# Optimization experiments

Measured on AMD Instinct MI355X. Metric: run time of the kernel, lower is better.

## Reference

```python
import jax, jax.numpy as jnp
import numpy as np

WORD, D, H = 512, 64, 8  # word_size, embed_dim (per-head), n_query

def setup_inputs() -> dict:
    key = jax.random.key(0)
    ks = jax.random.split(key, 9)
    B, S = 2, 4096
    sw = 1.0 / np.sqrt(WORD)
    x  = jax.random.normal(ks[0], (B, S, WORD), dtype=jnp.float32)
    Wk = jax.random.normal(ks[1], (WORD, D), dtype=jnp.float32) * sw
    bk = jnp.zeros((D,), jnp.float32)
    Wv = jax.random.normal(ks[2], (WORD, D), dtype=jnp.float32) * sw
    bv = jnp.zeros((D,), jnp.float32)
    Wq = jax.random.normal(ks[3], (H, WORD, D), dtype=jnp.float32) * sw
    bq = jnp.zeros((H, D), jnp.float32)
    Wp = jax.random.normal(ks[4], (H * D, D), dtype=jnp.float32) * (1.0 / np.sqrt(H * D))
    bp = jnp.zeros((D,), jnp.float32)
    return {"x": x, "Wq": Wq, "bq": bq, "Wk": Wk, "bk": bk, "Wv": Wv, "bv": bv, "Wp": Wp, "bp": bp}

def reference(x, Wq, bq, Wk, bk, Wv, bv, Wp, bp):
    # shared K/V across all query heads (multi-query attention)
    K = x @ Wk + bk                                   # [b, s, d]
    V = x @ Wv + bv                                   # [b, s, d]
    Q = jnp.einsum('bsw,hwd->bhsd', x, Wq) + bq[None, :, None, :]  # [b, h, s, d]
    scale = 1.0 / jnp.sqrt(jnp.float32(D))
    scores = jnp.einsum('bhsd,btd->bhst', Q, K) * scale  # [b, h, s, t]
    attn = jax.nn.softmax(scores, axis=-1)
    Z = jnp.einsum('bhst,btd->bhsd', attn, V)            # [b, h, s, d]
    B, _, S, _ = Z.shape
    Zc = jnp.transpose(Z, (0, 2, 1, 3)).reshape(B, S, H * D)  # concat heads
    return Zc @ Wp + bp                                   # [b, s, d]
```

## Files before the change

### kernel.cpp

```cpp
#include <hip/hip_runtime.h>
#include <hip/hip_bf16.h>
#include <stdint.h>

#define BB 2
#define SS 4096
#define WW 512
#define DD 64
#define HH 8
#define QSCALE 0.1803368801111244f

typedef __hip_bfloat16 bf16;
typedef __bf16 bf16x8 __attribute__((ext_vector_type(8)));
typedef float f32x16 __attribute__((ext_vector_type(16)));
typedef unsigned int u32x4 __attribute__((ext_vector_type(4)));
typedef unsigned int u32x2 __attribute__((ext_vector_type(2)));

union U4 { u32x4 u4; unsigned int u[4]; bf16x8 v; };

__device__ __forceinline__ float ldv(const float* p, size_t i) { return p[i]; }
__device__ __forceinline__ float ldv(const bf16* p, size_t i)  { return __bfloat162float(p[i]); }

__device__ __forceinline__ unsigned short f2bu(float f) {
    union Ub { bf16 b; unsigned short u; } t;
    t.b = __float2bfloat16(f);
    return t.u;
}

__device__ __forceinline__ float fast_exp2(float x) {
#if __has_builtin(__builtin_amdgcn_exp2f)
    return __builtin_amdgcn_exp2f(x);
#else
    return exp2f(x);
#endif
}

__device__ __forceinline__ f32x16 mfma_bf16(bf16x8 a, bf16x8 b, f32x16 c) {
    return __builtin_amdgcn_mfma_f32_32x32x16_bf16(a, b, c, 0, 0, 0);
}

__device__ __forceinline__ unsigned int pk_bf16(float lo, float hi) {
    unsigned int a = __float_as_uint(lo) + 0x8000u;
    unsigned int b = __float_as_uint(hi) + 0x8000u;
    return __builtin_amdgcn_perm(b, a, 0x07060302u);
}

__device__ __forceinline__ unsigned int cvtpk_bf16(float lo, float hi) {
    unsigned int r;
    asm("v_cvt_pk_bf16_f32 %0, %1, %2" : "=v"(r) : "v"(lo), "v"(hi));
    return r;
}

__device__ __forceinline__ int block_detect(const void* raw, int* cntLds)
{
    if (threadIdx.x == 0) *cntLds = 0;
    __syncthreads();
    const bf16* xb = (const bf16*)raw;
    const float v = __bfloat162float(xb[2 * threadIdx.x]);
    const float a = fabsf(v);
    const bool insane = !(v == v) || (a >= 1.0e4f) || (a != 0.0f && a <= 1.0e-8f);
    const unsigned long long m = __ballot(insane);
    if ((threadIdx.x & 63) == 0) atomicAdd(cntLds, __popcll(m));
    __syncthreads();
    return (*cntLds * 2 > 256) ? 1 : 0;
}

template<typename T>
__device__ __forceinline__ void prep_w_body(
    const T* Wq, const T* bq, const T* Wk, const T* bk,
    const T* Wv, const T* bv, const T* Wp, const T* bp,
    unsigned short* Wb, float* bb, float (*Tt)[65], int pwblk)
{
    const int tid = threadIdx.x;
    const int cg = pwblk >> 3, wg = pwblk & 7;
    const int c0 = cg * 64, w0 = wg * 64;
    const T* src = (cg == 0) ? Wk : (cg == 1) ? Wv
                 : (cg == 10) ? Wp : (Wq + (size_t)(cg - 2) * WW * DD);
    const float scale = (cg >= 2 && cg < 10) ? QSCALE : 1.0f;

    #pragma unroll
    for (int i = 0; i < 16; ++i) {
        const int e = i * 256 + tid, w = e >> 6, d = e & 63;
        Tt[w][d] = ldv(src, (size_t)(w0 + w) * DD + d) * scale;
    }
    __syncthreads();
    #pragma unroll
    for (int i = 0; i < 16; ++i) {
        const int e = i * 256 + tid, d = e >> 6, w = e & 63;
        Wb[(size_t)(c0 + d) * WW + w0 + w] = f2bu(Tt[w][d]);
    }
    if (pwblk == 0) {
        #pragma unroll
        for (int i = 0; i < 3; ++i) {
            const int c = tid + i * 256;
            if (c < 704) {
                float v;
                if (c < 64)       v = ldv(bk, c);
                else if (c < 128) v = ldv(bv, c - 64);
                else if (c < 640) v = ldv(bq, c - 128) * QSCALE;
                else              v = ldv(bp, c - 640);
                bb[c] = v;
            }
        }
    }
}

__global__ __launch_bounds__(256) void prep_kernel(
    const void* x, const void* Wq, const void* bq, const void* Wk, const void* bk,
    const void* Wv, const void* bv, const void* Wp, const void* bp,
    unsigned short* xb, unsigned short* Wb, float* bb, int* flag)
{
    __shared__ float Tt[64][65];
    __shared__ int cnt;
    const int blk = blockIdx.x;

    if (blk < 2048) {
        const int fl = block_detect(x, &cnt);
        if (blk == 0 && threadIdx.x == 0) *flag = fl;
        const size_t i = ((size_t)blk * 256 + threadIdx.x) * 8;
        if (fl) {
            const float4* p = (const float4*)((const float*)x + i);
            const float4 a = p[0], b = p[1];
            unsigned int w[4];
            w[0] = pk_bf16(a.x, a.y); w[1] = pk_bf16(a.z, a.w);
            w[2] = pk_bf16(b.x, b.y); w[3] = pk_bf16(b.z, b.w);
            *(u32x4*)(xb + i) = *(u32x4*)w;
        } else {
            *(u32x4*)(xb + i) = *(const u32x4*)((const unsigned short*)x + i);
        }
    } else {
        const int fl = block_detect(Wk, &cnt);
        if (fl)
            prep_w_body<float>((const float*)Wq, (const float*)bq, (const float*)Wk,
                               (const float*)bk, (const float*)Wv, (const float*)bv,
                               (const float*)Wp, (const float*)bp, Wb, bb, Tt, blk - 2048);
        else
            prep_w_body<bf16>((const bf16*)Wq, (const bf16*)bq, (const bf16*)Wk,
                              (const bf16*)bk, (const bf16*)Wv, (const bf16*)bv,
                              (const bf16*)Wp, (const bf16*)bp, Wb, bb, Tt, blk - 2048);
    }
}

#define KP 40

__global__ __launch_bounds__(256, 2) void proj_mfma_kernel(
    const unsigned short* __restrict__ xb, const unsigned short* __restrict__ Wb,
    const float* __restrict__ bb,
    bf16* __restrict__ Kb, unsigned short* __restrict__ Vtg, bf16* __restrict__ Qb)
{
    __shared__ unsigned short As[2][128 * KP];
    __shared__ unsigned short Bs[2][128 * KP];

    const int tid = threadIdx.x;
    const int wv = tid >> 6, ln = tid & 63;
    const int g = ln >> 5, cc = ln & 31;
    const int nblk = blockIdx.x % 5, mblk = blockIdx.x / 5;
    const int row0 = mblk * 128, n0 = nblk * 128;
    const int wm = (wv & 1) * 64, wn = (wv >> 1) * 64;

    const int sm = tid >> 2;
    const int sko = (tid & 3) * 8;

    u32x4 pa[2], pb[2];
    #define GLOAD(kt)                                                          \
        do {                                                                   \
            _Pragma("unroll")                                                  \
            for (int i = 0; i < 2; ++i) {                                      \
                const int m = sm + i * 64;                                     \
                pa[i] = *(const u32x4*)&xb[(size_t)(row0 + m) * WW + (kt) * 32 + sko]; \
                pb[i] = *(const u32x4*)&Wb[(size_t)(n0 + m) * WW + (kt) * 32 + sko];   \
            }                                                                  \
        } while (0)
    #define LWRITE(buf)                                                        \
        do {                                                                   \
            _Pragma("unroll")                                                  \
            for (int i = 0; i < 2; ++i) {                                      \
                const int m = sm + i * 64;                                     \
                *(u32x4*)&As[buf][m * KP + sko] = pa[i];                       \
                *(u32x4*)&Bs[buf][m * KP + sko] = pb[i];                       \
            }                                                                  \
        } while (0)

    f32x16 acc[2][2];
    #pragma unroll
    for (int a = 0; a < 2; ++a)
        #pragma unroll
        for (int c2 = 0; c2 < 2; ++c2)
            #pragma unroll
            for (int i = 0; i < 16; ++i) acc[a][c2][i] = 0.f;

    GLOAD(0); LWRITE(0);
    GLOAD(1);

    for (int kt = 0; kt < 16; ++kt) {
        __syncthreads();
        const int buf = kt & 1;
        #pragma unroll
        for (int ks = 0; ks < 2; ++ks) {
            U4 af[2], bfr[2];
            #pragma unroll
            for (int ms = 0; ms < 2; ++ms)
                af[ms].u4 = *(const u32x4*)&As[buf][(wm + ms * 32 + cc) * KP + ks * 16 + g * 8];
            #pragma unroll
            for (int ns = 0; ns < 2; ++ns)
                bfr[ns].u4 = *(const u32x4*)&Bs[buf][(wn + ns * 32 + cc) * KP + ks * 16 + g * 8];
            #pragma unroll
            for (int ms = 0; ms < 2; ++ms)
                #pragma unroll
                for (int ns = 0; ns < 2; ++ns)
                    acc[ms][ns] = mfma_bf16(af[ms].v, bfr[ns].v, acc[ms][ns]);
        }
        if (kt < 15) {
            LWRITE(buf ^ 1);
            if (kt < 14) GLOAD(kt + 2);
        }
    }
    #undef GLOAD
    #undef LWRITE

    const int b = row0 >> 12;
    #pragma unroll
    for (int ns = 0; ns < 2; ++ns) {
        const int c = n0 + wn + ns * 32 + cc;
        const int grp = c >> 6, d = c & 63;
        const float bias = bb[c];
        if (grp == 1) {
            unsigned short* vt = Vtg + ((size_t)(b * DD + d)) * SS;
            #pragma unroll
            for (int ms = 0; ms < 2; ++ms) {
                #pragma unroll
                for (int reg = 0; reg < 16; ++reg) {
                    const int r = (reg & 3) + 8 * (reg >> 2) + 4 * g;
                    const int lrow = (row0 & 4095) + wm + ms * 32 + r;
                    const int srow = (lrow & ~12) | ((lrow & 4) << 1) | ((lrow & 8) >> 1);
                    vt[srow] = f2bu(acc[ms][ns][reg] + bias);
                }
            }
        } else {
            bf16* base = (grp == 0) ? Kb
                       : Qb + (size_t)((b * HH + grp - 2) - b) * SS * DD;
            #pragma unroll
            for (int ms = 0; ms < 2; ++ms) {
                #pragma unroll
                for (int reg = 0; reg < 16; ++reg) {
                    const int r = (reg & 3) + 8 * (reg >> 2) + 4 * g;
                    const int row = row0 + wm + ms * 32 + r;
                    base[(size_t)row * DD + d] = __float2bfloat16(acc[ms][ns][reg] + bias);
                }
            }
        }
    }
}

#define VTP 72
#define ZP_PART ((size_t)16 * 64 * 4096)
#define LP_PART ((size_t)16 * 4096)

template<int TSPLIT>
__global__ __launch_bounds__(256, 2) void attn_mfma_kernel(
    const bf16* __restrict__ Kb, const unsigned short* __restrict__ Vtg,
    const bf16* __restrict__ Qb, bf16* __restrict__ Zb,
    float* __restrict__ Zp, float* __restrict__ Lp)
{
    __shared__ unsigned short Vt[2][64 * VTP];
    __shared__ unsigned short Kt[2][64 * VTP];

    const int tid = threadIdx.x;
    const int wv = tid >> 6, ln = tid & 63;
    const int g  = ln >> 5, cc = ln & 31;
    constexpr int TSB = (TSPLIT == 1) ? 0 : 1;
    const int chunk = blockIdx.x & 15;
    const int tsp = (blockIdx.x >> 4) & (TSPLIT - 1);
    const int bh  = blockIdx.x >> (4 + TSB);
    const int b = bh >> 3, h = bh & 7;
    const int qw = chunk * 256 + wv * 64;
    const int it0 = tsp * (64 / TSPLIT);
    const int itN = it0 + 64 / TSPLIT;

    const unsigned short* Kg = (const unsigned short*)(Kb + (size_t)b * SS * DD);
    const unsigned short* Vg = Vtg + (size_t)b * DD * SS;
    const char* Qg = (const char*)(Qb + (size_t)(b * HH + h) * SS * DD);

    const int sr = tid >> 2, sc = (tid & 3) * 16;
    const unsigned short* VgRow = Vg + (size_t)sr * SS;

    U4 qf[2][4];
    #pragma unroll
    for (int nt = 0; nt < 2; ++nt)
        #pragma unroll
        for (int ks = 0; ks < 4; ++ks)
            qf[nt][ks].u4 = *(const u32x4*)(Qg +
                (size_t)((qw + nt * 32 + cc) * 64 + g * 8 + ks * 16) * 2);

    const f32x16 fzero = {0.f, 0.f, 0.f, 0.f, 0.f, 0.f, 0.f, 0.f,
                          0.f, 0.f, 0.f, 0.f, 0.f, 0.f, 0.f, 0.f};
    U4 ones;
    ones.u[0] = 0x3F803F80u; ones.u[1] = 0x3F803F80u;
    ones.u[2] = 0x3F803F80u; ones.u[3] = 0x3F803F80u;

    f32x16 zacc[2][2];
    #pragma unroll
    for (int nt = 0; nt < 2; ++nt)
        #pragma unroll
        for (int dt = 0; dt < 2; ++dt)
            #pragma unroll
            for (int i = 0; i < 16; ++i) zacc[nt][dt][i] = 0.f;

    f32x16 lacc[2];
    #pragma unroll
    for (int nt = 0; nt < 2; ++nt)
        #pragma unroll
        for (int i = 0; i < 16; ++i) lacc[nt][i] = 0.f;

    {
        const unsigned short* ksrc = Kg + (size_t)(it0 * 64 + sr) * 64 + sc;
        const unsigned short* vsrc = VgRow + it0 * 64 + sc;
        *(u32x4*)&Kt[0][sr * VTP + sc + 0] = *(const u32x4*)&ksrc[0];
        *(u32x4*)&Kt[0][sr * VTP + sc + 8] = *(const u32x4*)&ksrc[8];
        *(u32x4*)&Vt[0][sr * VTP + sc + 0] = *(const u32x4*)&vsrc[0];
        *(u32x4*)&Vt[0][sr * VTP + sc + 8] = *(const u32x4*)&vsrc[8];
    }

    for (int it = it0; it < itN; ++it) {
        __syncthreads();
        const int buf = it & 1;
        const bool more = (it + 1) < itN;
        u32x4 pk0, pk1, pv0, pv1;
        if (more) {
            const unsigned short* ksrc = Kg + (size_t)((it + 1) * 64 + sr) * 64 + sc;
            const unsigned short* vsrc = VgRow + (it + 1) * 64 + sc;
            pk0 = *(const u32x4*)&ksrc[0];
            pk1 = *(const u32x4*)&ksrc[8];
            pv0 = *(const u32x4*)&vsrc[0];
            pv1 = *(const u32x4*)&vsrc[8];
        }

        #pragma unroll
        for (int si = 0; si < 2; ++si) {
            U4 kf[4];
            #pragma unroll
            for (int ks = 0; ks < 4; ++ks)
                kf[ks].u4 = *(const u32x4*)&Kt[buf][(si * 32 + cc) * VTP +
                                                    ks * 16 + g * 8];
            U4 vf[2][2];
            #pragma unroll
            for (int ks = 0; ks < 2; ++ks)
                #pragma unroll
                for (int dt = 0; dt < 2; ++dt)
                    vf[ks][dt].u4 = *(const u32x4*)&Vt[buf][(dt * 32 + cc) * VTP +
                                                            si * 32 + ks * 16 + g * 8];

            #pragma unroll
            for (int nt = 0; nt < 2; ++nt) {
                __builtin_amdgcn_s_setprio(1);
                f32x16 s = mfma_bf16(kf[0].v, qf[nt][0].v, fzero);
                #pragma unroll
                for (int ks = 1; ks < 4; ++ks) s = mfma_bf16(kf[ks].v, qf[nt][ks].v, s);
                __builtin_amdgcn_s_setprio(0);

                float p[16];
                #pragma unroll
                for (int i = 0; i < 16; ++i) p[i] = fast_exp2(s[i]);
                unsigned int w0[8];
                #pragma unroll
                for (int i2 = 0; i2 < 8; ++i2)
                    w0[i2] = cvtpk_bf16(p[2 * i2], p[2 * i2 + 1]);

                __builtin_amdgcn_s_setprio(1);
                #pragma unroll
                for (int ks = 0; ks < 2; ++ks) {
                    U4 pb;
                    pb.u[0] = w0[ks * 4 + 0]; pb.u[1] = w0[ks * 4 + 1];
                    pb.u[2] = w0[ks * 4 + 2]; pb.u[3] = w0[ks * 4 + 3];
                    lacc[nt] = mfma_bf16(ones.v, pb.v, lacc[nt]);
                    #pragma unroll
                    for (int dt = 0; dt < 2; ++dt)
                        zacc[nt][dt] = mfma_bf16(vf[ks][dt].v, pb.v, zacc[nt][dt]);
                }
                __builtin_amdgcn_s_setprio(0);
            }
        }

        if (more) {
            *(u32x4*)&Kt[buf ^ 1][sr * VTP + sc + 0] = pk0;
            *(u32x4*)&Kt[buf ^ 1][sr * VTP + sc + 8] = pk1;
            *(u32x4*)&Vt[buf ^ 1][sr * VTP + sc + 0] = pv0;
            *(u32x4*)&Vt[buf ^ 1][sr * VTP + sc + 8] = pv1;
        }
    }

    float l[2];
    l[0] = lacc[0][0];
    l[1] = lacc[1][0];

    if (TSPLIT == 1) {
        #pragma unroll
        for (int nt = 0; nt < 2; ++nt) {
            const float rr = 1.0f / l[nt];
            bf16* zp = Zb + (size_t)(b * SS + qw + nt * 32 + cc) * (HH * DD)
                     + h * DD + g * 4;
            #pragma unroll
            for (int dt = 0; dt < 2; ++dt)
                #pragma unroll
                for (int i = 0; i < 16; ++i) {
                    const int d = (i & 3) + 8 * (i >> 2) + 32 * dt;
                    zp[d] = __float2bfloat16(zacc[nt][dt][i] * rr);
                }
        }
    } else {
        float* zp0 = Zp + (size_t)(tsp * 16 + bh) * (64 * 4096);
        #pragma unroll
        for (int nt = 0; nt < 2; ++nt) {
            const int q = qw + nt * 32 + cc;
            #pragma unroll
            for (int dt = 0; dt < 2; ++dt)
                #pragma unroll
                for (int i = 0; i < 16; ++i) {
                    const int d = (i & 3) + 8 * (i >> 2) + 4 * g + 32 * dt;
                    zp0[(size_t)d * 4096 + q] = zacc[nt][dt][i];
                }
            if (g == 0)
                Lp[(size_t)(tsp * 16 + bh) * 4096 + q] = l[nt];
        }
    }
}

template<int NP>
__global__ __launch_bounds__(256) void combine_kernel(
    const float* __restrict__ Zp, const float* __restrict__ Lp,
    bf16* __restrict__ Zb)
{
    const size_t T = (size_t)blockIdx.x * 256 + threadIdx.x;
    const int sblk = (int)(T & 511);
    const int d  = (int)((T >> 9) & 63);
    const int bh = (int)(T >> 15);
    const int s0 = sblk * 8;
    const int b = bh >> 3, h = bh & 7;

    const float* p0 = Zp + ((size_t)bh * 64 + d) * 4096 + s0;
    const float* l0 = Lp + (size_t)bh * 4096 + s0;

    float z[8], lv[8];
    #pragma unroll
    for (int j = 0; j < 8; ++j) { z[j] = 0.f; lv[j] = 0.f; }
    #pragma unroll
    for (int np = 0; np < NP; ++np) {
        const float* p = p0 + (size_t)np * ZP_PART;
        const float* l = l0 + (size_t)np * LP_PART;
        #pragma unroll
        for (int j = 0; j < 8; j += 4) {
            const float4 a = *(const float4*)(p + j);
            z[j] += a.x; z[j+1] += a.y; z[j+2] += a.z; z[j+3] += a.w;
            const float4 e = *(const float4*)(l + j);
            lv[j] += e.x; lv[j+1] += e.y; lv[j+2] += e.z; lv[j+3] += e.w;
        }
    }
    bf16* zo = Zb + ((size_t)(b * SS + s0)) * (HH * DD) + h * DD + d;
    #pragma unroll
    for (int j = 0; j < 8; ++j)
        zo[(size_t)j * (HH * DD)] = __float2bfloat16(z[j] / lv[j]);
}

__global__ __launch_bounds__(256) void outp_mfma_kernel(
    const bf16* __restrict__ Zb, const unsigned short* __restrict__ Wb,
    const float* __restrict__ bb, const int* flag, void* out)
{
    __shared__ unsigned short As[2][128 * KP];
    __shared__ unsigned short Bs[2][64 * KP];

    const int tid = threadIdx.x;
    const int wv = tid >> 6, ln = tid & 63;
    const int g = ln >> 5, cc = ln & 31;
    const int row0 = blockIdx.x * 128;
    const int sm = tid >> 2, sko = (tid & 3) * 8;

    const unsigned short* Zu = (const unsigned short*)Zb;
    const unsigned short* Wn = Wb + (size_t)640 * WW;
    const float* bbp = bb + 640;

    u32x4 pa[2], pbv;
    #define GLOAD2(kt)                                                         \
        do {                                                                   \
            _Pragma("unroll")                                                  \
            for (int i = 0; i < 2; ++i)                                        \
                pa[i] = *(const u32x4*)&Zu[(size_t)(row0 + sm + i * 64) * WW + (kt) * 32 + sko]; \
            pbv = *(const u32x4*)&Wn[(size_t)sm * WW + (kt) * 32 + sko];       \
        } while (0)
    #define LWRITE2(buf)                                                       \
        do {                                                                   \
            _Pragma("unroll")                                                  \
            for (int i = 0; i < 2; ++i)                                        \
                *(u32x4*)&As[buf][(sm + i * 64) * KP + sko] = pa[i];           \
            *(u32x4*)&Bs[buf][sm * KP + sko] = pbv;                            \
        } while (0)

    f32x16 acc[2];
    #pragma unroll
    for (int ns = 0; ns < 2; ++ns)
        #pragma unroll
        for (int i = 0; i < 16; ++i) acc[ns][i] = 0.f;

    GLOAD2(0); LWRITE2(0);
    GLOAD2(1);

    for (int kt = 0; kt < 16; ++kt) {
        __syncthreads();
        const int buf = kt & 1;
        #pragma unroll
        for (int ks = 0; ks < 2; ++ks) {
            U4 af;
            af.u4 = *(const u32x4*)&As[buf][(wv * 32 + cc) * KP + ks * 16 + g * 8];
            #pragma unroll
            for (int ns = 0; ns < 2; ++ns) {
                U4 bf2;
                bf2.u4 = *(const u32x4*)&Bs[buf][(ns * 32 + cc) * KP + ks * 16 + g * 8];
                acc[ns] = mfma_bf16(af.v, bf2.v, acc[ns]);
            }
        }
        if (kt < 15) {
            LWRITE2(buf ^ 1);
            if (kt < 14) GLOAD2(kt + 2);
        }
    }
    #undef GLOAD2
    #undef LWRITE2

    const int fl = *flag;
    #pragma unroll
    for (int ns = 0; ns < 2; ++ns) {
        const int c = ns * 32 + cc;
        const float bias = bbp[c];
        #pragma unroll
        for (int reg = 0; reg < 16; ++reg) {
            const int r = (reg & 3) + 8 * (reg >> 2) + 4 * g;
            const int row = row0 + wv * 32 + r;
            const float v = acc[ns][reg] + bias;
            if (fl) ((float*)out)[(size_t)row * DD + c] = v;
            else    ((bf16*)out)[(size_t)row * DD + c] = __float2bfloat16(v);
        }
    }
}

extern "C" void kernel_launch(void* const* d_in, const int* in_sizes, int n_in,
                              void* d_out, int out_size, void* d_ws, size_t ws_size,
                              hipStream_t stream)
{
    const void* x  = d_in[0];
    const void* Wq = d_in[1];
    const void* bq = d_in[2];
    const void* Wk = d_in[3];
    const void* bk = d_in[4];
    const void* Wv = d_in[5];
    const void* bv = d_in[6];
    const void* Wp = d_in[7];
    const void* bp = d_in[8];

    char* ws = (char*)d_ws;
    bf16* Kb = (bf16*)(ws);
    bf16* Qb = (bf16*)(ws + (2u << 20));
    bf16* Zb = (bf16*)(ws + (10u << 20));
    unsigned short* xb = (unsigned short*)(ws + (10u << 20));
    int* flag = (int*)(ws + (18u << 20));
    unsigned short* Wb = (unsigned short*)(ws + (18u << 20) + 64);
    float* bb = (float*)(ws + (18u << 20) + 64 + 704 * 512 * 2);
    unsigned short* Vtg = (unsigned short*)(ws + (19u << 20));
    float* Zp = (float*)(ws + (20u << 20));
    float* Lp = (float*)(ws + (20u << 20) + 2 * ZP_PART * 4);

    const size_t ws_need2 = (20u << 20) + (size_t)2 * ZP_PART * 4 + (size_t)2 * LP_PART * 4;

    prep_kernel<<<2136, 256, 0, stream>>>(x, Wq, bq, Wk, bk, Wv, bv, Wp, bp,
                                          xb, Wb, bb, flag);
    proj_mfma_kernel<<<320, 256, 0, stream>>>(xb, Wb, bb, Kb, Vtg, Qb);
    if (ws_size >= ws_need2) {
        attn_mfma_kernel<2><<<512, 256, 0, stream>>>(Kb, Vtg, Qb, Zb, Zp, Lp);
        combine_kernel<2><<<2048, 256, 0, stream>>>(Zp, Lp, Zb);
    } else {
        attn_mfma_kernel<1><<<256, 256, 0, stream>>>(Kb, Vtg, Qb, Zb, Zp, Lp);
    }
    outp_mfma_kernel<<<64, 256, 0, stream>>>(Zb, Wb, bb, flag, d_out);
}
```

Measured before the change: 198.6 us.

## Fuse split-K combine into output projection and halve its row tile

Removes the separate combine kernel. The output-projection GEMM now reads the two partial Z buffers and the softmax denominators directly, sums and normalizes them, and converts to bf16 while loading its A tile. This saves one launch and the round trip through the bf16 Z buffer. The row tile shrinks from 128 to 64 with a 2x2 wave layout, which doubles the grid to 128 blocks. The fused loads are strided by 4096 floats per d element, so they are uncoalesced scalar reads that could slow the GEMM's load phase.

```diff
diff --git a/kernel.cpp b/kernel.cpp
--- a/kernel.cpp
+++ b/kernel.cpp
@@ -424,80 +424,64 @@
     }
 }
 
-template<int NP>
-__global__ __launch_bounds__(256) void combine_kernel(
+template<int FUSED>
+__global__ __launch_bounds__(256) void outp_mfma_kernel(
+    const bf16* __restrict__ Zb,
     const float* __restrict__ Zp, const float* __restrict__ Lp,
-    bf16* __restrict__ Zb)
-{
-    const size_t T = (size_t)blockIdx.x * 256 + threadIdx.x;
-    const int sblk = (int)(T & 511);
-    const int d  = (int)((T >> 9) & 63);
-    const int bh = (int)(T >> 15);
-    const int s0 = sblk * 8;
-    const int b = bh >> 3, h = bh & 7;
-
-    const float* p0 = Zp + ((size_t)bh * 64 + d) * 4096 + s0;
-    const float* l0 = Lp + (size_t)bh * 4096 + s0;
-
-    float z[8], lv[8];
-    #pragma unroll
-    for (int j = 0; j < 8; ++j) { z[j] = 0.f; lv[j] = 0.f; }
-    #pragma unroll
-    for (int np = 0; np < NP; ++np) {
-        const float* p = p0 + (size_t)np * ZP_PART;
-        const float* l = l0 + (size_t)np * LP_PART;
-        #pragma unroll
-        for (int j = 0; j < 8; j += 4) {
-            const float4 a = *(const float4*)(p + j);
-            z[j] += a.x; z[j+1] += a.y; z[j+2] += a.z; z[j+3] += a.w;
-            const float4 e = *(const float4*)(l + j);
-            lv[j] += e.x; lv[j+1] += e.y; lv[j+2] += e.z; lv[j+3] += e.w;
-        }
-    }
-    bf16* zo = Zb + ((size_t)(b * SS + s0)) * (HH * DD) + h * DD + d;
-    #pragma unroll
-    for (int j = 0; j < 8; ++j)
-        zo[(size_t)j * (HH * DD)] = __float2bfloat16(z[j] / lv[j]);
-}
-
-__global__ __launch_bounds__(256) void outp_mfma_kernel(
-    const bf16* __restrict__ Zb, const unsigned short* __restrict__ Wb,
+    const unsigned short* __restrict__ Wb,
     const float* __restrict__ bb, const int* flag, void* out)
 {
-    __shared__ unsigned short As[2][128 * KP];
+    __shared__ unsigned short As[2][64 * KP];
     __shared__ unsigned short Bs[2][64 * KP];
 
     const int tid = threadIdx.x;
     const int wv = tid >> 6, ln = tid & 63;
     const int g = ln >> 5, cc = ln & 31;
-    const int row0 = blockIdx.x * 128;
+    const int wr = wv >> 1, wc = wv & 1;
+    const int row0 = blockIdx.x * 64;
     const int sm = tid >> 2, sko = (tid & 3) * 8;
 
     const unsigned short* Zu = (const unsigned short*)Zb;
     const unsigned short* Wn = Wb + (size_t)640 * WW;
     const float* bbp = bb + 640;
 
-    u32x4 pa[2], pbv;
+    const int srow = (row0 & 4095) + sm;
+    const int boff = (row0 >> 12) * 8;
+
+    u32x4 pa, pbv;
     #define GLOAD2(kt)                                                         \
         do {                                                                   \
-            _Pragma("unroll")                                                  \
-            for (int i = 0; i < 2; ++i)                                        \
-                pa[i] = *(const u32x4*)&Zu[(size_t)(row0 + sm + i * 64) * WW + (kt) * 32 + sko]; \
+            if (FUSED) {                                                       \
+                const int hh = (kt) >> 1;                                      \
+                const int d0 = ((kt) & 1) * 32 + sko;                          \
+                const size_t lbase = (size_t)(boff + hh) * 4096 + srow;        \
+                const float ls = Lp[lbase] + Lp[LP_PART + lbase];              \
+                const float rr = 1.0f / ls;                                    \
+                const float* zq0 = Zp + ((size_t)((boff + hh) * 64 + d0)) * 4096 + srow; \
+                unsigned int w[4];                                             \
+                _Pragma("unroll")                                              \
+                for (int j = 0; j < 4; ++j) {                                  \
+                    const float a0 = (zq0[(size_t)(2*j) * 4096] +              \
+                                      zq0[ZP_PART + (size_t)(2*j) * 4096]) * rr; \
+                    const float a1 = (zq0[(size_t)(2*j+1) * 4096] +            \
+                                      zq0[ZP_PART + (size_t)(2*j+1) * 4096]) * rr; \
+                    w[j] = cvtpk_bf16(a0, a1);                                 \
+                }                                                              \
+                pa = *(u32x4*)w;                                               \
+            } else {                                                           \
+                pa = *(const u32x4*)&Zu[(size_t)(row0 + sm) * WW + (kt) * 32 + sko]; \
+            }                                                                  \
             pbv = *(const u32x4*)&Wn[(size_t)sm * WW + (kt) * 32 + sko];       \
         } while (0)
     #define LWRITE2(buf)                                                       \
         do {                                                                   \
-            _Pragma("unroll")                                                  \
-            for (int i = 0; i < 2; ++i)                                        \
-                *(u32x4*)&As[buf][(sm + i * 64) * KP + sko] = pa[i];           \
+            *(u32x4*)&As[buf][sm * KP + sko] = pa;                             \
             *(u32x4*)&Bs[buf][sm * KP + sko] = pbv;                            \
         } while (0)
 
-    f32x16 acc[2];
-    #pragma unroll
-    for (int ns = 0; ns < 2; ++ns)
-        #pragma unroll
-        for (int i = 0; i < 16; ++i) acc[ns][i] = 0.f;
+    f32x16 acc;
+    #pragma unroll
+    for (int i = 0; i < 16; ++i) acc[i] = 0.f;
 
     GLOAD2(0); LWRITE2(0);
     GLOAD2(1);
@@ -507,14 +491,10 @@
         const int buf = kt & 1;
         #pragma unroll
         for (int ks = 0; ks < 2; ++ks) {
-            U4 af;
-            af.u4 = *(const u32x4*)&As[buf][(wv * 32 + cc) * KP + ks * 16 + g * 8];
-            #pragma unroll
-            for (int ns = 0; ns < 2; ++ns) {
-                U4 bf2;
-                bf2.u4 = *(const u32x4*)&Bs[buf][(ns * 32 + cc) * KP + ks * 16 + g * 8];
-                acc[ns] = mfma_bf16(af.v, bf2.v, acc[ns]);
-            }
+            U4 af, bf2;
+            af.u4  = *(const u32x4*)&As[buf][(wr * 32 + cc) * KP + ks * 16 + g * 8];
+            bf2.u4 = *(const u32x4*)&Bs[buf][(wc * 32 + cc) * KP + ks * 16 + g * 8];
+            acc = mfma_bf16(af.v, bf2.v, acc);
         }
         if (kt < 15) {
             LWRITE2(buf ^ 1);
@@ -525,18 +505,15 @@
     #undef LWRITE2
 
     const int fl = *flag;
-    #pragma unroll
-    for (int ns = 0; ns < 2; ++ns) {
-        const int c = ns * 32 + cc;
-        const float bias = bbp[c];
-        #pragma unroll
-        for (int reg = 0; reg < 16; ++reg) {
-            const int r = (reg & 3) + 8 * (reg >> 2) + 4 * g;
-            const int row = row0 + wv * 32 + r;
-            const float v = acc[ns][reg] + bias;
-            if (fl) ((float*)out)[(size_t)row * DD + c] = v;
-            else    ((bf16*)out)[(size_t)row * DD + c] = __float2bfloat16(v);
-        }
+    const int c = wc * 32 + cc;
+    const float bias = bbp[c];
+    #pragma unroll
+    for (int reg = 0; reg < 16; ++reg) {
+        const int r = (reg & 3) + 8 * (reg >> 2) + 4 * g;
+        const int row = row0 + wr * 32 + r;
+        const float v = acc[reg] + bias;
+        if (fl) ((float*)out)[(size_t)row * DD + c] = v;
+        else    ((bf16*)out)[(size_t)row * DD + c] = __float2bfloat16(v);
     }
 }
 
@@ -573,9 +550,9 @@
     proj_mfma_kernel<<<320, 256, 0, stream>>>(xb, Wb, bb, Kb, Vtg, Qb);
     if (ws_size >= ws_need2) {
         attn_mfma_kernel<2><<<512, 256, 0, stream>>>(Kb, Vtg, Qb, Zb, Zp, Lp);
-        combine_kernel<2><<<2048, 256, 0, stream>>>(Zp, Lp, Zb);
+        outp_mfma_kernel<1><<<128, 256, 0, stream>>>(Zb, Zp, Lp, Wb, bb, flag, d_out);
     } else {
         attn_mfma_kernel<1><<<256, 256, 0, stream>>>(Kb, Vtg, Qb, Zb, Zp, Lp);
-    }
-    outp_mfma_kernel<<<64, 256, 0, stream>>>(Zb, Wb, bb, flag, d_out);
-}
+        outp_mfma_kernel<0><<<128, 256, 0, stream>>>(Zb, Zp, Lp, Wb, bb, flag, d_out);
+    }
+}
```

After: 182.8 us (median of 3 runs). -8.0%, faster.
